# Optimization experiments

Hardware: AMD Instinct MI355X
Metric: run time of the kernel (lower is better)

Reference implementation:

```python
import jax, jax.numpy as jnp
import numpy as np

B, L, D, R = 8, 2048, 512, 512  # batch, seq, feature, n_rules


def setup_inputs() -> dict:
    key = jax.random.key(0)
    ks = jax.random.split(key, 6)
    query = jax.random.normal(ks[0], (B, L, D), dtype=jnp.float32)
    # to_q: Linear(D, D)
    Wq = jax.random.normal(ks[1], (D, D), dtype=jnp.float32) / np.sqrt(D)
    bq = jnp.zeros((D,), dtype=jnp.float32)
    # to_c: Linear(L, R)
    Wc = jax.random.normal(ks[2], (R, L), dtype=jnp.float32) / np.sqrt(L)
    bc = jnp.zeros((R,), dtype=jnp.float32)
    # fuzzy rule params, torch.rand init (uniform [0,1)); widths kept away from 0
    centers = jax.random.uniform(ks[3], (R, D), dtype=jnp.float32)
    widths = jax.random.uniform(ks[4], (R, D), dtype=jnp.float32, minval=0.1, maxval=1.0)
    return {"query": query, "Wq": Wq, "bq": bq, "Wc": Wc, "bc": bc,
            "centers": centers, "widths": widths}


def reference(query, Wq, bq, Wc, bc, centers, widths):
    # q = to_q(query)  (projection=True)
    q = query @ Wq.T + bq  # (B, L, D)
    # z[b,l,r] = -0.5 * mean_d (|q - c| / w)^2 ; abs is a no-op under the square,
    # so expand (q - c)^2 / w^2 into three GEMM-friendly terms (exact same math).
    inv_w2 = 1.0 / (widths * widths)                      # (R, D)
    qq = (q * q) @ inv_w2.T                               # (B, L, R)
    qc = q @ (centers * inv_w2).T                         # (B, L, R)
    cc = jnp.sum(centers * centers * inv_w2, axis=-1)     # (R,)
    z = -(0.5 / D) * (qq - 2.0 * qc + cc)                 # (B, L, R)
    Fss = jax.nn.softmax(z, axis=-1)                      # (B, L, R); dropout p=0
    # conq = to_c applied along the L axis of query, yielding (B, R, D)
    conq = jnp.einsum('bld,rl->brd', query, Wc) + bc[None, :, None]
    return Fss @ conq                                     # (B, L, D)
```

## Files before the change

### kernel.cpp

```cpp
#include <hip/hip_runtime.h>
#include <hip/hip_bf16.h>

constexpr int Bb = 8, Ls = 2048, Dd = 512, Rr = 512;
constexpr int M1 = Bb * Ls;

typedef _Float16 h8v __attribute__((ext_vector_type(8)));
typedef _Float16 h4v __attribute__((ext_vector_type(4)));
typedef float f4v __attribute__((ext_vector_type(4)));

__device__ __forceinline__ void async_copy16(const void* g, void* l) {
  __builtin_amdgcn_global_load_lds((const __attribute__((address_space(1))) unsigned int*)g,
                                   (__attribute__((address_space(3))) unsigned int*)l, 16, 0, 0);
}

__device__ __forceinline__ void swizzle_xy(int& x, int& yy) {
  const int NX = gridDim.x;
  const int lin = ((int)blockIdx.z * (int)gridDim.y + (int)blockIdx.y) * NX + (int)blockIdx.x;
  const int xcd = lin & 7;
  const int w = lin >> 3;
  x = w % NX;
  yy = (w / NX) * 8 + xcd;
}

__global__ __launch_bounds__(256) void prep_all(
    const float* __restrict__ q, _Float16* __restrict__ qs, _Float16* __restrict__ qt,
    const float* __restrict__ Wq, _Float16* __restrict__ wq,
    const float* __restrict__ Wc, _Float16* __restrict__ wc,
    const float* __restrict__ centers, const float* __restrict__ widths,
    _Float16* __restrict__ iwh, _Float16* __restrict__ c2h, float* __restrict__ cc) {
  const int bid = blockIdx.x, tid = threadIdx.x;
  if (bid < 2048) {
    __shared__ float t[64][65];
    const int b = bid >> 8;
    const int l0 = ((bid >> 3) & 31) * 64;
    const int d0 = (bid & 7) * 64;
    const int r = tid >> 4, c4 = (tid & 15) * 4;
#pragma unroll
    for (int i = 0; i < 4; ++i) {
      const int l = r + i * 16;
      const float4 v = *(const float4*)&q[((long)b * Ls + l0 + l) * Dd + d0 + c4];
      t[l][c4] = v.x; t[l][c4 + 1] = v.y; t[l][c4 + 2] = v.z; t[l][c4 + 3] = v.w;
      h4v h = {(_Float16)v.x, (_Float16)v.y, (_Float16)v.z, (_Float16)v.w};
      *(h4v*)&qs[((long)b * Ls + l0 + l) * Dd + d0 + c4] = h;
    }
    __syncthreads();
#pragma unroll
    for (int i = 0; i < 4; ++i) {
      const int d = r + i * 16;
      h4v h = {(_Float16)t[c4][d], (_Float16)t[c4 + 1][d],
               (_Float16)t[c4 + 2][d], (_Float16)t[c4 + 3][d]};
      *(h4v*)&qt[((long)b * Dd + d0 + d) * Ls + l0 + c4] = h;
    }
  } else if (bid < 2304) {
    const int i = (bid - 2048) * 256 + tid;
    float4 v = *(const float4*)&Wq[(long)i * 4];
    h4v o = {(_Float16)v.x, (_Float16)v.y, (_Float16)v.z, (_Float16)v.w};
    *(h4v*)&wq[(long)i * 4] = o;
  } else if (bid < 3328) {
    const int i = (bid - 2304) * 256 + tid;
    float4 v = *(const float4*)&Wc[(long)i * 4];
    h4v o = {(_Float16)v.x, (_Float16)v.y, (_Float16)v.z, (_Float16)v.w};
    *(h4v*)&wc[(long)i * 4] = o;
  } else {
    const int wave = tid >> 6, lane = tid & 63;
    const int r = (bid - 3328) * 4 + wave;
    float s = 0.f;
#pragma unroll
    for (int j = 0; j < 8; ++j) {
      const int d = j * 64 + lane;
      const float c = centers[(long)r * Dd + d];
      const float w = widths[(long)r * Dd + d];
      const float iw = 1.0f / (w * w);
      iwh[(long)r * Dd + d] = (_Float16)iw;
      c2h[(long)r * Dd + d] = (_Float16)(-2.0f * c * iw);
      s += c * c * iw;
    }
#pragma unroll
    for (int o = 32; o > 0; o >>= 1) s += __shfl_xor(s, o, 64);
    if (lane == 0) cc[r] = s;
  }
}

__global__ __launch_bounds__(256) void reduce_cq(const float* __restrict__ p0,
                                                 const float* __restrict__ p1,
                                                 const float* __restrict__ bc,
                                                 _Float16* __restrict__ d, int n4) {
  int i = blockIdx.x * 256 + threadIdx.x;
  if (i < n4) {
    float4 a = *(const float4*)&p0[(long)i * 4];
    float4 b = *(const float4*)&p1[(long)i * 4];
    int c = (i * 4) & 511;
    h4v o = {(_Float16)(a.x + b.x + bc[c]), (_Float16)(a.y + b.y + bc[c + 1]),
             (_Float16)(a.z + b.z + bc[c + 2]), (_Float16)(a.w + b.w + bc[c + 3])};
    *(h4v*)&d[(long)i * 4] = o;
  }
}

template <int AI, int EPI>
__global__ __launch_bounds__(256) void gemm_h(
    const _Float16* __restrict__ A, const _Float16* __restrict__ Bm,
    const float* __restrict__ bias, float* __restrict__ Cf,
    _Float16* __restrict__ Ch, int Kext, int ldA, int ldB, int ldC, int kstep,
    long sA, long sB, long sC) {
  constexpr int TM = AI * 32;
  __shared__ _Float16 As[TM * 32];
  __shared__ _Float16 Bs[128 * 32];
  int x, yy;
  swizzle_xy(x, yy);
  const int y = yy % (int)gridDim.y;
  const int zz = yy / (int)gridDim.y;
  const int n0 = x * 128;
  const int m0 = y * TM;
  const int kb = zz * kstep;
  const _Float16* Ab = A + (long)zz * sA;
  const _Float16* Bb = Bm + (long)zz * sB;

  const int tid = threadIdx.x;
  const int wave = tid >> 6, lane = tid & 63;
  const int wm = wave >> 1, wn = wave & 1;
  const int quad = lane >> 4, tr = lane & 15;
  const int lrow = lane >> 2;
  const int lcol = (lane & 3) * 8;

  f4v acc[AI][4];
#pragma unroll
  for (int i = 0; i < AI; ++i)
#pragma unroll
    for (int j = 0; j < 4; ++j) acc[i][j] = (f4v){0.f, 0.f, 0.f, 0.f};

  for (int k0 = 0; k0 < Kext; k0 += 32) {
    __syncthreads();
#pragma unroll
    for (int c = wave; c < TM / 16; c += 4) {
      const long g = (long)(m0 + c * 16 + lrow) * ldA + kb + k0 + lcol;
      async_copy16(Ab + g, As + c * 512);
    }
#pragma unroll
    for (int c = wave; c < 8; c += 4) {
      const long g = (long)(n0 + c * 16 + lrow) * ldB + kb + k0 + lcol;
      async_copy16(Bb + g, Bs + c * 512);
    }
    __syncthreads();

    h8v af[AI], bf[4];
#pragma unroll
    for (int i = 0; i < AI; ++i)
      af[i] = *(const h8v*)&As[(wm * (AI * 16) + i * 16 + tr) * 32 + quad * 8];
#pragma unroll
    for (int j = 0; j < 4; ++j)
      bf[j] = *(const h8v*)&Bs[(wn * 64 + j * 16 + tr) * 32 + quad * 8];
#pragma unroll
    for (int i = 0; i < AI; ++i)
#pragma unroll
      for (int j = 0; j < 4; ++j)
        acc[i][j] = __builtin_amdgcn_mfma_f32_16x16x32_f16(af[i], bf[j], acc[i][j], 0, 0, 0);
  }

  float* Cfb = Cf ? Cf + (long)zz * sC : nullptr;
  _Float16* Chb = Ch ? Ch + (long)zz * sC : nullptr;
#pragma unroll
  for (int i = 0; i < AI; ++i)
#pragma unroll
    for (int j = 0; j < 4; ++j) {
      const int rbase = m0 + wm * (AI * 16) + i * 16 + quad * 4;
      const int cg = n0 + wn * 64 + j * 16 + tr;
#pragma unroll
      for (int r = 0; r < 4; ++r) {
        const float v = acc[i][j][r];
        const long row = rbase + r;
        if (EPI == 2) {
          Chb[row * (long)ldC + cg] = (_Float16)(v + bias[cg]);
        } else if (EPI == 3) {
          Cfb[row * (long)ldC + cg] = v;
        }
      }
    }
}

__global__ __launch_bounds__(256) void zq_gemm(
    const _Float16* __restrict__ Q, const _Float16* __restrict__ Iw,
    const _Float16* __restrict__ C2, const float* __restrict__ cc,
    float* __restrict__ Z) {
  __shared__ _Float16 As[128 * 32];
  __shared__ _Float16 B1[128 * 32];
  __shared__ _Float16 B2[128 * 32];
  int x, yy;
  swizzle_xy(x, yy);
  const int n0 = x * 128;
  const int m0 = yy * 128;

  const int tid = threadIdx.x;
  const int wave = tid >> 6, lane = tid & 63;
  const int wm = wave >> 1, wn = wave & 1;
  const int quad = lane >> 4, tr = lane & 15;
  const int lrow = lane >> 2;
  const int lcol = (lane & 3) * 8;

  f4v acc[4][4];
#pragma unroll
  for (int i = 0; i < 4; ++i)
#pragma unroll
    for (int j = 0; j < 4; ++j) acc[i][j] = (f4v){0.f, 0.f, 0.f, 0.f};

  for (int k0 = 0; k0 < 512; k0 += 32) {
    __syncthreads();
#pragma unroll
    for (int c = wave; c < 8; c += 4) {
      const long ga = (long)(m0 + c * 16 + lrow) * 512 + k0 + lcol;
      async_copy16(Q + ga, As + c * 512);
      const long gb = (long)(n0 + c * 16 + lrow) * 512 + k0 + lcol;
      async_copy16(Iw + gb, B1 + c * 512);
      async_copy16(C2 + gb, B2 + c * 512);
    }
    __syncthreads();

    h8v af[4], af2[4], b1[4], b2[4];
#pragma unroll
    for (int i = 0; i < 4; ++i) {
      af[i] = *(const h8v*)&As[(wm * 64 + i * 16 + tr) * 32 + quad * 8];
      af2[i] = af[i] * af[i];
    }
#pragma unroll
    for (int j = 0; j < 4; ++j) {
      b1[j] = *(const h8v*)&B1[(wn * 64 + j * 16 + tr) * 32 + quad * 8];
      b2[j] = *(const h8v*)&B2[(wn * 64 + j * 16 + tr) * 32 + quad * 8];
    }
#pragma unroll
    for (int i = 0; i < 4; ++i)
#pragma unroll
      for (int j = 0; j < 4; ++j) {
        acc[i][j] = __builtin_amdgcn_mfma_f32_16x16x32_f16(af2[i], b1[j], acc[i][j], 0, 0, 0);
        acc[i][j] = __builtin_amdgcn_mfma_f32_16x16x32_f16(af[i], b2[j], acc[i][j], 0, 0, 0);
      }
  }

  constexpr float zs = -0.0009765625f;
#pragma unroll
  for (int i = 0; i < 4; ++i)
#pragma unroll
    for (int j = 0; j < 4; ++j) {
      const int rbase = m0 + wm * 64 + i * 16 + quad * 4;
      const int cg = n0 + wn * 64 + j * 16 + tr;
      const float ccv = cc[cg];
#pragma unroll
      for (int r = 0; r < 4; ++r)
        Z[(long)(rbase + r) * 512 + cg] = (acc[i][j][r] + ccv) * zs;
    }
}

__global__ __launch_bounds__(256) void softmax_h(const float* __restrict__ Z,
                                                 _Float16* __restrict__ F) {
  const int wave = threadIdx.x >> 6;
  const int lane = threadIdx.x & 63;
  const long row = (long)blockIdx.x * 4 + wave;
  const float* p = Z + row * Rr;
  float4 v0 = *(const float4*)&p[lane * 8];
  float4 v1 = *(const float4*)&p[lane * 8 + 4];
  float v[8] = {v0.x, v0.y, v0.z, v0.w, v1.x, v1.y, v1.z, v1.w};
  float m = v[0];
#pragma unroll
  for (int i = 1; i < 8; ++i) m = fmaxf(m, v[i]);
#pragma unroll
  for (int s = 32; s > 0; s >>= 1) m = fmaxf(m, __shfl_xor(m, s, 64));
  float sum = 0.f;
#pragma unroll
  for (int i = 0; i < 8; ++i) {
    v[i] = __expf(v[i] - m);
    sum += v[i];
  }
#pragma unroll
  for (int s = 32; s > 0; s >>= 1) sum += __shfl_xor(sum, s, 64);
  const float inv = 1.0f / sum;
  h8v o;
#pragma unroll
  for (int i = 0; i < 8; ++i) o[i] = (_Float16)(v[i] * inv);
  *(h8v*)&F[row * Rr + lane * 8] = o;
}

extern "C" void kernel_launch(void* const* d_in, const int* in_sizes, int n_in,
                              void* d_out, int out_size, void* d_ws, size_t ws_size,
                              hipStream_t stream) {
  const float* query   = (const float*)d_in[0];
  const float* Wq      = (const float*)d_in[1];
  const float* bq      = (const float*)d_in[2];
  const float* Wc      = (const float*)d_in[3];
  const float* bc      = (const float*)d_in[4];
  const float* centers = (const float*)d_in[5];
  const float* widths  = (const float*)d_in[6];
  float* out = (float*)d_out;

  char* base = (char*)d_ws;
  auto alloc = [&](size_t bytes) {
    char* p = base;
    base += (bytes + 255) & ~(size_t)255;
    return p;
  };
  _Float16* qs  = (_Float16*)alloc((size_t)M1 * Dd * 2);
  _Float16* qt  = (_Float16*)alloc((size_t)M1 * Dd * 2);
  _Float16* q16 = (_Float16*)alloc((size_t)M1 * Dd * 2);
  float*    z   = (float*)alloc((size_t)M1 * Rr * 4);
  _Float16* fs  = (_Float16*)alloc((size_t)M1 * Rr * 2);
  _Float16* wq  = (_Float16*)alloc((size_t)Dd * Dd * 2);
  _Float16* wc  = (_Float16*)alloc((size_t)Rr * Ls * 2);
  _Float16* iwh = (_Float16*)alloc((size_t)Rr * Dd * 2);
  _Float16* c2h = (_Float16*)alloc((size_t)Rr * Dd * 2);
  float*    cc  = (float*)alloc((size_t)Rr * 4);
  _Float16* cq  = (_Float16*)alloc((size_t)Bb * Dd * Rr * 2);

  float* cqp = z;

  prep_all<<<3456, 256, 0, stream>>>(query, qs, qt, Wq, wq, Wc, wc,
                                     centers, widths, iwh, c2h, cc);

  gemm_h<4, 2><<<dim3(Dd / 128, M1 / 128, 1), 256, 0, stream>>>(
      qs, wq, bq, nullptr, q16, Dd, Dd, Dd, Dd, 0, 0, 0, 0);

  zq_gemm<<<dim3(Rr / 128, M1 / 128, 1), 256, 0, stream>>>(q16, iwh, c2h, cc, z);

  softmax_h<<<M1 / 4, 256, 0, stream>>>(z, fs);

  gemm_h<2, 3><<<dim3(Rr / 128, (Bb * Dd) / 64, 2), 256, 0, stream>>>(
      qt, wc, nullptr, cqp, nullptr, 1024, Ls, Ls, Rr, 1024,
      0, 0, (long)Bb * Dd * Rr);
  reduce_cq<<<(Bb * Dd * Rr / 4 + 255) / 256, 256, 0, stream>>>(
      cqp, cqp + (long)Bb * Dd * Rr, bc, cq, Bb * Dd * Rr / 4);

  gemm_h<4, 3><<<dim3(Dd / 128, Ls / 128, Bb), 256, 0, stream>>>(
      fs, cq, nullptr, out, nullptr, Rr, Rr, Rr, Dd, 0,
      (long)Ls * Rr, (long)Dd * Rr, (long)Ls * Dd);
}
```

Baseline: 190.1 us.

## Use 8-wave blocks for GEMMs and store logits in fp16

All GEMM kernels now launch 512 threads (8 waves) per 128-wide tile. Each wave covers half as many output columns, which cuts accumulator registers per wave and adds waves for latency hiding. The z logits are written as fp16 instead of fp32, halving the traffic between zq_gemm and softmax at some cost in logit precision. The cq partial buffer gets its own workspace allocation instead of aliasing z, since z is now too small to hold it.

```diff
diff --git a/kernel.cpp b/kernel.cpp
--- a/kernel.cpp
+++ b/kernel.cpp
@@ -96,13 +96,13 @@
   }
 }
 
-template <int AI, int EPI>
-__global__ __launch_bounds__(256) void gemm_h(
+template <int WM, int EPI>
+__global__ __launch_bounds__(512, 4) void gemm_h(
     const _Float16* __restrict__ A, const _Float16* __restrict__ Bm,
     const float* __restrict__ bias, float* __restrict__ Cf,
     _Float16* __restrict__ Ch, int Kext, int ldA, int ldB, int ldC, int kstep,
     long sA, long sB, long sC) {
-  constexpr int TM = AI * 32;
+  constexpr int TM = WM * 32;
   __shared__ _Float16 As[TM * 32];
   __shared__ _Float16 Bs[128 * 32];
   int x, yy;
@@ -117,53 +117,53 @@
 
   const int tid = threadIdx.x;
   const int wave = tid >> 6, lane = tid & 63;
-  const int wm = wave >> 1, wn = wave & 1;
+  const int wm = wave >> 2, wn = wave & 3;
   const int quad = lane >> 4, tr = lane & 15;
   const int lrow = lane >> 2;
   const int lcol = (lane & 3) * 8;
 
-  f4v acc[AI][4];
-#pragma unroll
-  for (int i = 0; i < AI; ++i)
-#pragma unroll
-    for (int j = 0; j < 4; ++j) acc[i][j] = (f4v){0.f, 0.f, 0.f, 0.f};
+  f4v acc[WM][2];
+#pragma unroll
+  for (int i = 0; i < WM; ++i)
+#pragma unroll
+    for (int j = 0; j < 2; ++j) acc[i][j] = (f4v){0.f, 0.f, 0.f, 0.f};
 
   for (int k0 = 0; k0 < Kext; k0 += 32) {
     __syncthreads();
 #pragma unroll
-    for (int c = wave; c < TM / 16; c += 4) {
+    for (int c = wave; c < TM / 16; c += 8) {
       const long g = (long)(m0 + c * 16 + lrow) * ldA + kb + k0 + lcol;
       async_copy16(Ab + g, As + c * 512);
     }
 #pragma unroll
-    for (int c = wave; c < 8; c += 4) {
+    for (int c = wave; c < 8; c += 8) {
       const long g = (long)(n0 + c * 16 + lrow) * ldB + kb + k0 + lcol;
       async_copy16(Bb + g, Bs + c * 512);
     }
     __syncthreads();
 
-    h8v af[AI], bf[4];
-#pragma unroll
-    for (int i = 0; i < AI; ++i)
-      af[i] = *(const h8v*)&As[(wm * (AI * 16) + i * 16 + tr) * 32 + quad * 8];
-#pragma unroll
-    for (int j = 0; j < 4; ++j)
-      bf[j] = *(const h8v*)&Bs[(wn * 64 + j * 16 + tr) * 32 + quad * 8];
-#pragma unroll
-    for (int i = 0; i < AI; ++i)
-#pragma unroll
-      for (int j = 0; j < 4; ++j)
+    h8v af[WM], bf[2];
+#pragma unroll
+    for (int i = 0; i < WM; ++i)
+      af[i] = *(const h8v*)&As[(wm * (WM * 16) + i * 16 + tr) * 32 + quad * 8];
+#pragma unroll
+    for (int j = 0; j < 2; ++j)
+      bf[j] = *(const h8v*)&Bs[(wn * 32 + j * 16 + tr) * 32 + quad * 8];
+#pragma unroll
+    for (int i = 0; i < WM; ++i)
+#pragma unroll
+      for (int j = 0; j < 2; ++j)
         acc[i][j] = __builtin_amdgcn_mfma_f32_16x16x32_f16(af[i], bf[j], acc[i][j], 0, 0, 0);
   }
 
   float* Cfb = Cf ? Cf + (long)zz * sC : nullptr;
   _Float16* Chb = Ch ? Ch + (long)zz * sC : nullptr;
 #pragma unroll
-  for (int i = 0; i < AI; ++i)
-#pragma unroll
-    for (int j = 0; j < 4; ++j) {
-      const int rbase = m0 + wm * (AI * 16) + i * 16 + quad * 4;
-      const int cg = n0 + wn * 64 + j * 16 + tr;
+  for (int i = 0; i < WM; ++i)
+#pragma unroll
+    for (int j = 0; j < 2; ++j) {
+      const int rbase = m0 + wm * (WM * 16) + i * 16 + quad * 4;
+      const int cg = n0 + wn * 32 + j * 16 + tr;
 #pragma unroll
       for (int r = 0; r < 4; ++r) {
         const float v = acc[i][j][r];
@@ -177,10 +177,10 @@
     }
 }
 
-__global__ __launch_bounds__(256) void zq_gemm(
+__global__ __launch_bounds__(512, 4) void zq_gemm(
     const _Float16* __restrict__ Q, const _Float16* __restrict__ Iw,
     const _Float16* __restrict__ C2, const float* __restrict__ cc,
-    float* __restrict__ Z) {
+    _Float16* __restrict__ Zh) {
   __shared__ _Float16 As[128 * 32];
   __shared__ _Float16 B1[128 * 32];
   __shared__ _Float16 B2[128 * 32];
@@ -191,44 +191,43 @@
 
   const int tid = threadIdx.x;
   const int wave = tid >> 6, lane = tid & 63;
-  const int wm = wave >> 1, wn = wave & 1;
+  const int wm = wave >> 2, wn = wave & 3;
   const int quad = lane >> 4, tr = lane & 15;
   const int lrow = lane >> 2;
   const int lcol = (lane & 3) * 8;
 
-  f4v acc[4][4];
+  f4v acc[4][2];
 #pragma unroll
   for (int i = 0; i < 4; ++i)
 #pragma unroll
-    for (int j = 0; j < 4; ++j) acc[i][j] = (f4v){0.f, 0.f, 0.f, 0.f};
+    for (int j = 0; j < 2; ++j) acc[i][j] = (f4v){0.f, 0.f, 0.f, 0.f};
 
   for (int k0 = 0; k0 < 512; k0 += 32) {
     __syncthreads();
-#pragma unroll
-    for (int c = wave; c < 8; c += 4) {
-      const long ga = (long)(m0 + c * 16 + lrow) * 512 + k0 + lcol;
-      async_copy16(Q + ga, As + c * 512);
-      const long gb = (long)(n0 + c * 16 + lrow) * 512 + k0 + lcol;
-      async_copy16(Iw + gb, B1 + c * 512);
-      async_copy16(C2 + gb, B2 + c * 512);
-    }
-    __syncthreads();
-
-    h8v af[4], af2[4], b1[4], b2[4];
+    {
+      const long ga = (long)(m0 + wave * 16 + lrow) * 512 + k0 + lcol;
+      async_copy16(Q + ga, As + wave * 512);
+      const long gb = (long)(n0 + wave * 16 + lrow) * 512 + k0 + lcol;
+      async_copy16(Iw + gb, B1 + wave * 512);
+      async_copy16(C2 + gb, B2 + wave * 512);
+    }
+    __syncthreads();
+
+    h8v af[4], af2[4], b1[2], b2[2];
 #pragma unroll
     for (int i = 0; i < 4; ++i) {
       af[i] = *(const h8v*)&As[(wm * 64 + i * 16 + tr) * 32 + quad * 8];
       af2[i] = af[i] * af[i];
     }
 #pragma unroll
-    for (int j = 0; j < 4; ++j) {
-      b1[j] = *(const h8v*)&B1[(wn * 64 + j * 16 + tr) * 32 + quad * 8];
-      b2[j] = *(const h8v*)&B2[(wn * 64 + j * 16 + tr) * 32 + quad * 8];
+    for (int j = 0; j < 2; ++j) {
+      b1[j] = *(const h8v*)&B1[(wn * 32 + j * 16 + tr) * 32 + quad * 8];
+      b2[j] = *(const h8v*)&B2[(wn * 32 + j * 16 + tr) * 32 + quad * 8];
     }
 #pragma unroll
     for (int i = 0; i < 4; ++i)
 #pragma unroll
-      for (int j = 0; j < 4; ++j) {
+      for (int j = 0; j < 2; ++j) {
         acc[i][j] = __builtin_amdgcn_mfma_f32_16x16x32_f16(af2[i], b1[j], acc[i][j], 0, 0, 0);
         acc[i][j] = __builtin_amdgcn_mfma_f32_16x16x32_f16(af[i], b2[j], acc[i][j], 0, 0, 0);
       }
@@ -238,25 +237,25 @@
 #pragma unroll
   for (int i = 0; i < 4; ++i)
 #pragma unroll
-    for (int j = 0; j < 4; ++j) {
+    for (int j = 0; j < 2; ++j) {
       const int rbase = m0 + wm * 64 + i * 16 + quad * 4;
-      const int cg = n0 + wn * 64 + j * 16 + tr;
+      const int cg = n0 + wn * 32 + j * 16 + tr;
       const float ccv = cc[cg];
 #pragma unroll
       for (int r = 0; r < 4; ++r)
-        Z[(long)(rbase + r) * 512 + cg] = (acc[i][j][r] + ccv) * zs;
-    }
-}
-
-__global__ __launch_bounds__(256) void softmax_h(const float* __restrict__ Z,
+        Zh[(long)(rbase + r) * 512 + cg] = (_Float16)((acc[i][j][r] + ccv) * zs);
+    }
+}
+
+__global__ __launch_bounds__(256) void softmax_h(const _Float16* __restrict__ Zh,
                                                  _Float16* __restrict__ F) {
   const int wave = threadIdx.x >> 6;
   const int lane = threadIdx.x & 63;
   const long row = (long)blockIdx.x * 4 + wave;
-  const float* p = Z + row * Rr;
-  float4 v0 = *(const float4*)&p[lane * 8];
-  float4 v1 = *(const float4*)&p[lane * 8 + 4];
-  float v[8] = {v0.x, v0.y, v0.z, v0.w, v1.x, v1.y, v1.z, v1.w};
+  h8v zv = *(const h8v*)&Zh[row * Rr + lane * 8];
+  float v[8];
+#pragma unroll
+  for (int i = 0; i < 8; ++i) v[i] = (float)zv[i];
   float m = v[0];
 #pragma unroll
   for (int i = 1; i < 8; ++i) m = fmaxf(m, v[i]);
@@ -298,34 +297,33 @@
   _Float16* qs  = (_Float16*)alloc((size_t)M1 * Dd * 2);
   _Float16* qt  = (_Float16*)alloc((size_t)M1 * Dd * 2);
   _Float16* q16 = (_Float16*)alloc((size_t)M1 * Dd * 2);
-  float*    z   = (float*)alloc((size_t)M1 * Rr * 4);
+  _Float16* zh  = (_Float16*)alloc((size_t)M1 * Rr * 2);
   _Float16* fs  = (_Float16*)alloc((size_t)M1 * Rr * 2);
   _Float16* wq  = (_Float16*)alloc((size_t)Dd * Dd * 2);
   _Float16* wc  = (_Float16*)alloc((size_t)Rr * Ls * 2);
   _Float16* iwh = (_Float16*)alloc((size_t)Rr * Dd * 2);
   _Float16* c2h = (_Float16*)alloc((size_t)Rr * Dd * 2);
   float*    cc  = (float*)alloc((size_t)Rr * 4);
+  float*    cqp = (float*)alloc((size_t)2 * Bb * Dd * Rr * 4);
   _Float16* cq  = (_Float16*)alloc((size_t)Bb * Dd * Rr * 2);
-
-  float* cqp = z;
 
   prep_all<<<3456, 256, 0, stream>>>(query, qs, qt, Wq, wq, Wc, wc,
                                      centers, widths, iwh, c2h, cc);
 
-  gemm_h<4, 2><<<dim3(Dd / 128, M1 / 128, 1), 256, 0, stream>>>(
+  gemm_h<4, 2><<<dim3(Dd / 128, M1 / 128, 1), 512, 0, stream>>>(
       qs, wq, bq, nullptr, q16, Dd, Dd, Dd, Dd, 0, 0, 0, 0);
 
-  zq_gemm<<<dim3(Rr / 128, M1 / 128, 1), 256, 0, stream>>>(q16, iwh, c2h, cc, z);
-
-  softmax_h<<<M1 / 4, 256, 0, stream>>>(z, fs);
-
-  gemm_h<2, 3><<<dim3(Rr / 128, (Bb * Dd) / 64, 2), 256, 0, stream>>>(
+  zq_gemm<<<dim3(Rr / 128, M1 / 128, 1), 512, 0, stream>>>(q16, iwh, c2h, cc, zh);
+
+  softmax_h<<<M1 / 4, 256, 0, stream>>>(zh, fs);
+
+  gemm_h<2, 3><<<dim3(Rr / 128, (Bb * Dd) / 64, 2), 512, 0, stream>>>(
       qt, wc, nullptr, cqp, nullptr, 1024, Ls, Ls, Rr, 1024,
       0, 0, (long)Bb * Dd * Rr);
   reduce_cq<<<(Bb * Dd * Rr / 4 + 255) / 256, 256, 0, stream>>>(
       cqp, cqp + (long)Bb * Dd * Rr, bc, cq, Bb * Dd * Rr / 4);
 
-  gemm_h<4, 3><<<dim3(Dd / 128, Ls / 128, Bb), 256, 0, stream>>>(
+  gemm_h<4, 3><<<dim3(Dd / 128, Ls / 128, Bb), 512, 0, stream>>>(
       fs, cq, nullptr, out, nullptr, Rr, Rr, Rr, Dd, 0,
       (long)Ls * Rr, (long)Dd * Rr, (long)Ls * Dd);
 }
```

Result: no change. 187.6 us (-1.3%).
